# Kernel tuning notes

Measured on AMD Instinct MI355X. Metric: run time of the kernel, lower is better.

Reference implementation:

```python
import jax, jax.numpy as jnp
import numpy as np

TEMPERATURE = 0.07
ALPHA = 1.0
SIGMOID_SCALE = 1.0
EPS = 1e-8

BSZ, N_VIEWS, D = 256, 2, 128


def setup_inputs() -> dict:
    key = jax.random.key(0)
    k1, k2, k3 = jax.random.split(key, 3)
    features = jax.random.normal(k1, (BSZ, N_VIEWS, D), dtype=jnp.float32)
    labels = jax.random.uniform(k2, (BSZ,), dtype=jnp.float32)  # continuous positions
    v_prog = jax.random.normal(k3, (D,), dtype=jnp.float32)     # learned direction param
    return {"features": features, "labels": labels, "v_prog": v_prog}


def _l2_normalize(x, axis, eps=1e-12):
    # matches F.normalize: x / clamp_min(||x||, eps)
    n = jnp.linalg.norm(x, axis=axis, keepdims=True)
    return x / jnp.maximum(n, eps)


def reference(features, labels, v_prog):
    bsz, n_views, d = features.shape
    # contrast_mode='all': torch.cat(torch.unbind(features, dim=1), dim=0)
    cf = jnp.concatenate([features[:, v] for v in range(n_views)], axis=0)  # (n, d)
    pos = jnp.tile(labels.reshape(-1, 1), (n_views, 1))                      # (n, 1)
    n = cf.shape[0]

    # ---------------- RAL loss ----------------
    f = _l2_normalize(cf, axis=1)
    sim = (f @ f.T) / TEMPERATURE                 # (n, n)
    pd = jnp.abs(pos - pos.T)                     # (n, n) |p_i - p_j|
    exp_sim = jnp.exp(sim)
    not_i = ~jnp.eye(n, dtype=bool)               # exclude k == i
    # mask3[i, j, k] = (pd[i,k] >= pd[i,j]) & (k != i)
    mask3 = (pd[:, None, :] >= pd[:, :, None]) & not_i[:, None, :]
    # denominator[i, j] = sum_k exp_sim[i, k] * mask3[i, j, k]  (fused masked reduction)
    denom = jnp.sum(jnp.where(mask3, exp_sim[:, None, :], 0.0), axis=2)
    loss_mat = -jnp.log(exp_sim / (denom + EPS))
    valid = not_i.astype(jnp.float32) * (denom > 0).astype(jnp.float32)
    soft_w = jax.nn.sigmoid(SIGMOID_SCALE * pd)   # apply_soft_weights=True
    cnt = valid.sum()
    ral = jnp.where(cnt > 0, (loss_mat * soft_w * valid).sum() / cnt, 0.0)

    # ---------------- OAL loss ----------------
    v = v_prog / (jnp.linalg.norm(v_prog) + EPS)
    mask = (pos < pos.T).astype(jnp.float32)      # mask[i,j] = p_i < p_j
    # cos[i,j] = (f_j - f_i) . v / ||f_j - f_i|| computed in O(n^2) without (n,n,d)
    proj = cf @ v                                  # (n,)
    sqn = jnp.sum(cf * cf, axis=1)                 # (n,)
    sqdist = jnp.maximum(sqn[:, None] + sqn[None, :] - 2.0 * (cf @ cf.T), 0.0)
    dist = jnp.sqrt(jnp.maximum(sqdist, 1e-24))    # clamp matches F.normalize eps behaviour
    cos = (proj[None, :] - proj[:, None]) / jnp.maximum(dist, 1e-12)
    cm = mask.sum()
    oal = jnp.where(cm > 0, -(cos * mask).sum() / cm, 0.0)

    return ral + ALPHA * oal
```

## Files before the change

kernel.cpp:

```cpp
#include <hip/hip_runtime.h>
#include <math.h>

#define NN 512
#define DD 128
#define TEMP_INV (1.0f / 0.07f)
#define EPSF 1e-8f

#define WS_VN   15
#define WS_SV   16
#define WS_RK   528
#define WS_PROJ 1040
#define WS_SQN  1552
#define WS_PART 2064
#define WS_G    4096

__global__ __launch_bounds__(256) void prep_kernel(
    const float* __restrict__ features,
    const float* __restrict__ labels,
    const float* __restrict__ v_prog,
    float* __restrict__ ws)
{
    const int b = blockIdx.x;
    const int t = threadIdx.x;
    if (b < 1024) {
        __shared__ __align__(16) float a_s[16 * 132];
        __shared__ __align__(16) float b_s[16 * 132];
        const int tr = b >> 5, tc = b & 31;
        {
            const int rl = t >> 5, q = t & 31;
            const int ra0 = 16 * tr + rl, rb0 = 16 * tc + rl;
            const int ra1 = ra0 + 8,      rb1 = rb0 + 8;
            float4 va0 = ((const float4*)features)[((ra0 & 255) * 2 + (ra0 >> 8)) * 32 + q];
            float4 vb0 = ((const float4*)features)[((rb0 & 255) * 2 + (rb0 >> 8)) * 32 + q];
            float4 va1 = ((const float4*)features)[((ra1 & 255) * 2 + (ra1 >> 8)) * 32 + q];
            float4 vb1 = ((const float4*)features)[((rb1 & 255) * 2 + (rb1 >> 8)) * 32 + q];
            *(float4*)(a_s + (rl + 0) * 132 + 4 * q) = va0;
            *(float4*)(b_s + (rl + 0) * 132 + 4 * q) = vb0;
            *(float4*)(a_s + (rl + 8) * 132 + 4 * q) = va1;
            *(float4*)(b_s + (rl + 8) * 132 + 4 * q) = vb1;
        }
        __syncthreads();
        const int y = t >> 4, x = t & 15;
        const float4* arow = (const float4*)(a_s + y * 132);
        const float4* brow = (const float4*)(b_s + x * 132);
        float c0 = 0.f, c1 = 0.f, c2 = 0.f, c3 = 0.f;
        #pragma unroll 8
        for (int q = 0; q < 32; ++q) {
            float4 a = arow[q]; float4 v = brow[q];
            c0 += a.x * v.x; c1 += a.y * v.y; c2 += a.z * v.z; c3 += a.w * v.w;
        }
        const float c = (c0 + c1) + (c2 + c3);
        const int gr = 16 * tr + y, gc = 16 * tc + x;
        ws[WS_G + gr * NN + gc] = c;
        if (gr == gc) ws[WS_SQN + gr] = c;
    } else if (b < 1026) {
        __shared__ __align__(16) float vp_s[DD];
        if (t < DD) vp_s[t] = v_prog[t];
        __syncthreads();
        const int row = (b - 1024) * 256 + t;
        const float4* src = (const float4*)features + ((row & 255) * 2 + (row >> 8)) * 32;
        const float4* v4 = (const float4*)vp_s;
        float p0 = 0.f, p1 = 0.f, p2 = 0.f, p3 = 0.f;
        #pragma unroll 8
        for (int q = 0; q < 32; ++q) {
            float4 a = src[q]; float4 v = v4[q];
            p0 += a.x*v.x; p1 += a.y*v.y; p2 += a.z*v.z; p3 += a.w*v.w;
        }
        ws[WS_PROJ + row] = (p0 + p1) + (p2 + p3);
    } else if (b == 1026) {
        __shared__ float s0[4];
        float x = (t < DD) ? v_prog[t] : 0.f;
        float s = x * x;
        #pragma unroll
        for (int o = 32; o > 0; o >>= 1) s += __shfl_down(s, o);
        if ((t & 63) == 0) s0[t >> 6] = s;
        __syncthreads();
        if (t == 0) ws[WS_VN] = sqrtf(s0[0] + s0[1] + s0[2] + s0[3]) + EPSF;
    } else {
        __shared__ __align__(16) float pos_s[NN];
        const int k = (b - 1027) * 256 + t;
        for (int m = t; m < NN; m += 256) pos_s[m] = labels[m & 255];
        __syncthreads();
        const float pk = pos_s[k];
        const float4* p4 = (const float4*)pos_s;
        int r = 0;
        #pragma unroll 8
        for (int q = 0; q < NN / 4; ++q) {
            float4 v = p4[q];
            const int m0 = 4 * q;
            r += (int)(v.x < pk) | ((int)(v.x == pk) & (int)(m0 + 0 < k));
            r += (int)(v.y < pk) | ((int)(v.y == pk) & (int)(m0 + 1 < k));
            r += (int)(v.z < pk) | ((int)(v.z == pk) & (int)(m0 + 2 < k));
            r += (int)(v.w < pk) | ((int)(v.w == pk) & (int)(m0 + 3 < k));
        }
        ws[WS_SV + r] = pk;
        ((int*)ws)[WS_RK + k] = r;
    }
}

__global__ __launch_bounds__(512) void main_kernel(
    const float* __restrict__ labels,
    float* __restrict__ ws)
{
    __shared__ float sv_s[NN];
    __shared__ float esS[NN];
    __shared__ float wtot[8];
    __shared__ float red_s[32];

    const int i = blockIdx.x;
    const int t = threadIdx.x;

    sv_s[t] = ws[WS_SV + t];
    const int rk_t = ((const int*)ws)[WS_RK + t];
    const int rk_i = ((const int*)ws)[WS_RK + i];
    const float g      = ws[WS_G + i * NN + t];
    const float sqn_i  = ws[WS_SQN + i];
    const float sqn_k  = ws[WS_SQN + t];
    const float proj_i = ws[WS_PROJ + i];
    const float proj_k = ws[WS_PROJ + t];
    const float vn     = ws[WS_VN];
    const float pos_i  = labels[i & 255];
    const float pos_k  = labels[t & 255];

    const float inv_ni = 1.0f / fmaxf(sqrtf(sqn_i), 1e-12f);
    const float inv_nk = 1.0f / fmaxf(sqrtf(sqn_k), 1e-12f);
    const float sim    = g * inv_ni * inv_nk * TEMP_INV;
    const float es     = (t == i) ? 0.0f : __expf(sim);
    esS[rk_t] = es;

    float oal_sum = 0.f, oal_cnt = 0.f;
    if (pos_i < pos_k) {
        float sqd  = fmaxf(sqn_i + sqn_k - 2.0f * g, 0.0f);
        float dist = sqrtf(fmaxf(sqd, 1e-24f));
        oal_sum = (proj_k - proj_i) / (vn * fmaxf(dist, 1e-12f));
        oal_cnt = 1.0f;
    }
    __syncthreads();

    float s = esS[t];
    #pragma unroll
    for (int off = 1; off < 64; off <<= 1) {
        float u = __shfl_up(s, off);
        if ((t & 63) >= off) s += u;
    }
    const int wid = t >> 6;
    if ((t & 63) == 63) wtot[wid] = s;
    __syncthreads();
    float woff = 0.f;
    for (int w = 0; w < wid; ++w) woff += wtot[w];
    esS[t] = s + woff;
    __syncthreads();
    const float total = esS[NN - 1];

    const float thr = fabsf(pos_i - pos_k);
    int lo = 0, hi = rk_i;
    #pragma unroll
    for (int step = 256; step > 0; step >>= 1) {
        if (lo + step <= rk_i && !(fabsf(pos_i - sv_s[lo + step - 1]) < thr)) lo += step;
        if (hi + step <= NN   &&  (fabsf(pos_i - sv_s[hi + step - 1]) < thr)) hi += step;
    }

    const float pe_lo = (lo > 0) ? esS[lo - 1] : 0.0f;
    const float pe_hi = (hi > 0) ? esS[hi - 1] : 0.0f;
    float ral_sum = 0.f, ral_cnt = 0.f;
    if (t != i) {
        float denom = fmaxf(pe_lo + (total - pe_hi), es);
        const float sw = 1.0f / (1.0f + __expf(-thr));
        ral_sum = (__logf(denom + EPSF) - sim) * sw;
        ral_cnt = 1.0f;
    }

    #pragma unroll
    for (int o = 32; o > 0; o >>= 1) {
        ral_sum += __shfl_down(ral_sum, o);
        ral_cnt += __shfl_down(ral_cnt, o);
        oal_sum += __shfl_down(oal_sum, o);
        oal_cnt += __shfl_down(oal_cnt, o);
    }
    if ((t & 63) == 0) {
        red_s[wid*4+0] = ral_sum; red_s[wid*4+1] = ral_cnt;
        red_s[wid*4+2] = oal_sum; red_s[wid*4+3] = oal_cnt;
    }
    __syncthreads();
    if (t == 0) {
        float rs = 0.f, rc = 0.f, os = 0.f, oc = 0.f;
        #pragma unroll
        for (int w = 0; w < 8; ++w) {
            rs += red_s[w*4+0]; rc += red_s[w*4+1];
            os += red_s[w*4+2]; oc += red_s[w*4+3];
        }
        float* pp = ws + WS_PART + i * 4;
        pp[0] = rs; pp[1] = rc; pp[2] = os; pp[3] = oc;
    }
}

__global__ __launch_bounds__(256) void final_kernel(
    const float* __restrict__ ws, float* __restrict__ out)
{
    __shared__ double dred[16];
    const int t = threadIdx.x;
    double rs = 0.0, rc = 0.0, os = 0.0, oc = 0.0;
    for (int b = t; b < NN; b += 256) {
        const float* p = ws + WS_PART + b * 4;
        rs += (double)p[0]; rc += (double)p[1];
        os += (double)p[2]; oc += (double)p[3];
    }
    #pragma unroll
    for (int o = 32; o > 0; o >>= 1) {
        rs += __shfl_down(rs, o);
        rc += __shfl_down(rc, o);
        os += __shfl_down(os, o);
        oc += __shfl_down(oc, o);
    }
    if ((t & 63) == 0) {
        int w = t >> 6;
        dred[w*4+0] = rs; dred[w*4+1] = rc;
        dred[w*4+2] = os; dred[w*4+3] = oc;
    }
    __syncthreads();
    if (t == 0) {
        double RS = 0, RC = 0, OS = 0, OC = 0;
        for (int w = 0; w < 4; ++w) {
            RS += dred[w*4+0]; RC += dred[w*4+1];
            OS += dred[w*4+2]; OC += dred[w*4+3];
        }
        double ral = (RC > 0.0) ? RS / RC : 0.0;
        double oal = (OC > 0.0) ? -(OS / OC) : 0.0;
        out[0] = (float)(ral + oal);
    }
}

extern "C" void kernel_launch(void* const* d_in, const int* in_sizes, int n_in,
                              void* d_out, int out_size, void* d_ws, size_t ws_size,
                              hipStream_t stream) {
    const float* features = (const float*)d_in[0];
    const float* labels   = (const float*)d_in[1];
    const float* v_prog   = (const float*)d_in[2];
    float* ws  = (float*)d_ws;
    float* out = (float*)d_out;

    hipLaunchKernelGGL(prep_kernel,  dim3(1029), dim3(256), 0, stream,
                       features, labels, v_prog, ws);
    hipLaunchKernelGGL(main_kernel,  dim3(NN),   dim3(512), 0, stream, labels, ws);
    hipLaunchKernelGGL(final_kernel, dim3(1),    dim3(256), 0, stream, ws, out);
}
```

Measured before the change: 30.98 us.

## Fuse final reduction into main kernel via fixed-point atomics and last-block election

```diff
diff --git a/kernel.cpp b/kernel.cpp
--- a/kernel.cpp
+++ b/kernel.cpp
@@ -11,8 +11,10 @@
 #define WS_RK   528
 #define WS_PROJ 1040
 #define WS_SQN  1552
-#define WS_PART 2064
 #define WS_G    4096
+
+#define SCALE_RAL 268435456.0
+#define SCALE_OAL 8589934592.0
 
 __global__ __launch_bounds__(256) void prep_kernel(
     const float* __restrict__ features,
@@ -75,7 +77,11 @@
         for (int o = 32; o > 0; o >>= 1) s += __shfl_down(s, o);
         if ((t & 63) == 0) s0[t >> 6] = s;
         __syncthreads();
-        if (t == 0) ws[WS_VN] = sqrtf(s0[0] + s0[1] + s0[2] + s0[3]) + EPSF;
+        if (t == 0) {
+            ws[WS_VN] = sqrtf(s0[0] + s0[1] + s0[2] + s0[3]) + EPSF;
+            long long* acc = (long long*)ws;
+            acc[1] = 0; acc[2] = 0; acc[3] = 0; acc[4] = 0;
+        }
     } else {
         __shared__ __align__(16) float pos_s[NN];
         const int k = (b - 1027) * 256 + t;
@@ -100,12 +106,14 @@
 
 __global__ __launch_bounds__(512) void main_kernel(
     const float* __restrict__ labels,
-    float* __restrict__ ws)
+    float* __restrict__ ws,
+    float* __restrict__ out)
 {
     __shared__ float sv_s[NN];
     __shared__ float esS[NN];
     __shared__ float wtot[8];
     __shared__ float red_s[32];
+    __shared__ int is_last;
 
     const int i = blockIdx.x;
     const int t = threadIdx.x;
@@ -189,41 +197,23 @@
             rs += red_s[w*4+0]; rc += red_s[w*4+1];
             os += red_s[w*4+2]; oc += red_s[w*4+3];
         }
-        float* pp = ws + WS_PART + i * 4;
-        pp[0] = rs; pp[1] = rc; pp[2] = os; pp[3] = oc;
-    }
-}
-
-__global__ __launch_bounds__(256) void final_kernel(
-    const float* __restrict__ ws, float* __restrict__ out)
-{
-    __shared__ double dred[16];
-    const int t = threadIdx.x;
-    double rs = 0.0, rc = 0.0, os = 0.0, oc = 0.0;
-    for (int b = t; b < NN; b += 256) {
-        const float* p = ws + WS_PART + b * 4;
-        rs += (double)p[0]; rc += (double)p[1];
-        os += (double)p[2]; oc += (double)p[3];
-    }
-    #pragma unroll
-    for (int o = 32; o > 0; o >>= 1) {
-        rs += __shfl_down(rs, o);
-        rc += __shfl_down(rc, o);
-        os += __shfl_down(os, o);
-        oc += __shfl_down(oc, o);
-    }
-    if ((t & 63) == 0) {
-        int w = t >> 6;
-        dred[w*4+0] = rs; dred[w*4+1] = rc;
-        dred[w*4+2] = os; dred[w*4+3] = oc;
-    }
-    __syncthreads();
-    if (t == 0) {
-        double RS = 0, RC = 0, OS = 0, OC = 0;
-        for (int w = 0; w < 4; ++w) {
-            RS += dred[w*4+0]; RC += dred[w*4+1];
-            OS += dred[w*4+2]; OC += dred[w*4+3];
-        }
+        long long* acc = (long long*)ws;
+        __hip_atomic_fetch_add(&acc[1], llrint((double)rs * SCALE_RAL), __ATOMIC_RELAXED, __HIP_MEMORY_SCOPE_AGENT);
+        __hip_atomic_fetch_add(&acc[2], llrint((double)rc),             __ATOMIC_RELAXED, __HIP_MEMORY_SCOPE_AGENT);
+        __hip_atomic_fetch_add(&acc[3], llrint((double)os * SCALE_OAL), __ATOMIC_RELAXED, __HIP_MEMORY_SCOPE_AGENT);
+        __hip_atomic_fetch_add(&acc[4], llrint((double)oc),             __ATOMIC_RELAXED, __HIP_MEMORY_SCOPE_AGENT);
+        unsigned old = __hip_atomic_fetch_add((unsigned*)ws, 1u, __ATOMIC_ACQ_REL,
+                                              __HIP_MEMORY_SCOPE_AGENT);
+        is_last = ((old & (NN - 1u)) == NN - 1u);
+    }
+    __syncthreads();
+
+    if (is_last && t == 0) {
+        long long* acc = (long long*)ws;
+        double RS = (double)__hip_atomic_load(&acc[1], __ATOMIC_RELAXED, __HIP_MEMORY_SCOPE_AGENT) / SCALE_RAL;
+        double RC = (double)__hip_atomic_load(&acc[2], __ATOMIC_RELAXED, __HIP_MEMORY_SCOPE_AGENT);
+        double OS = (double)__hip_atomic_load(&acc[3], __ATOMIC_RELAXED, __HIP_MEMORY_SCOPE_AGENT) / SCALE_OAL;
+        double OC = (double)__hip_atomic_load(&acc[4], __ATOMIC_RELAXED, __HIP_MEMORY_SCOPE_AGENT);
         double ral = (RC > 0.0) ? RS / RC : 0.0;
         double oal = (OC > 0.0) ? -(OS / OC) : 0.0;
         out[0] = (float)(ral + oal);
@@ -239,8 +229,7 @@
     float* ws  = (float*)d_ws;
     float* out = (float*)d_out;
 
-    hipLaunchKernelGGL(prep_kernel,  dim3(1029), dim3(256), 0, stream,
+    hipLaunchKernelGGL(prep_kernel, dim3(1029), dim3(256), 0, stream,
                        features, labels, v_prog, ws);
-    hipLaunchKernelGGL(main_kernel,  dim3(NN),   dim3(512), 0, stream, labels, ws);
-    hipLaunchKernelGGL(final_kernel, dim3(1),    dim3(256), 0, stream, ws, out);
+    hipLaunchKernelGGL(main_kernel, dim3(NN),   dim3(512), 0, stream, labels, ws, out);
 }
```

After: 61.36 us. +98.1%, slower.
